# Kernel tuning notes

Hardware: AMD Instinct MI355X
Metric: run time of the kernel (lower is better)

Reference implementation:

```python
import jax, jax.numpy as jnp
import numpy as np

DIM = 128
NUM_HEADS = 8
HEAD_DIM = DIM // NUM_HEADS
N_NODES = 50000
N_EDGES = 800000


def setup_inputs() -> dict:
    key = jax.random.key(0)
    ks = jax.random.split(key, 10)
    scale = 1.0 / np.sqrt(DIM)
    x = jax.random.normal(ks[0], (N_NODES, DIM), dtype=jnp.float32)
    edge_index = jax.random.randint(ks[1], (2, N_EDGES), 0, N_NODES, dtype=jnp.int64)
    Wq = jax.random.normal(ks[2], (DIM, DIM), dtype=jnp.float32) * scale
    bq = jnp.zeros((DIM,), dtype=jnp.float32)
    Wk = jax.random.normal(ks[3], (DIM, DIM), dtype=jnp.float32) * scale
    bk = jnp.zeros((DIM,), dtype=jnp.float32)
    Wv = jax.random.normal(ks[4], (DIM, DIM), dtype=jnp.float32) * scale
    bv = jnp.zeros((DIM,), dtype=jnp.float32)
    Wo = jax.random.normal(ks[5], (DIM, DIM), dtype=jnp.float32) * scale
    bo = jnp.zeros((DIM,), dtype=jnp.float32)
    return {"x": x, "edge_index": edge_index, "Wq": Wq, "bq": bq,
            "Wk": Wk, "bk": bk, "Wv": Wv, "bv": bv, "Wo": Wo, "bo": bo}


def reference(x, edge_index, Wq, bq, Wk, bk, Wv, bv, Wo, bo):
    n = x.shape[0]
    tgt = edge_index[0]  # softmax group / scatter destination
    src = edge_index[1]  # gather source
    # projections: torch nn.Linear -> x @ W.T + b
    q = (x @ Wq.T + bq).reshape(n, NUM_HEADS, HEAD_DIM)
    k = (x @ Wk.T + bk).reshape(n, NUM_HEADS, HEAD_DIM)
    v = (x @ Wv.T + bv).reshape(n, NUM_HEADS, HEAD_DIM)
    # edge-wise attention scores: [E, H]
    scores = jnp.einsum('ehd,ehd->eh', q[src], k[tgt]) / np.sqrt(HEAD_DIM).astype(np.float32)
    # segment softmax over edges grouped by target node
    m = jax.ops.segment_max(scores, tgt, num_segments=n)          # [N, H]
    m = jax.lax.stop_gradient(m)
    p = jnp.exp(scores - m[tgt])                                   # [E, H]
    s = jax.ops.segment_sum(p, tgt, num_segments=n)               # [N, H]
    probs = p / s[tgt]
    # weighted scatter-add of source values
    weighted = v[src] * probs[..., None]                           # [E, H, D]
    agg = jax.ops.segment_sum(weighted, tgt, num_segments=n)      # [N, H, D]
    out = agg.reshape(n, DIM) @ Wo.T + bo
    # dropout is identity in eval mode
    return out
```

## Files before the change

### kernel.cpp

```cpp
#include <hip/hip_runtime.h>
#include <hip/hip_bf16.h>
#include <math.h>

#define NN 50000
#define NE 800000
#define DIM 128
#define NH 8
#define HD 16
#define NTILE 3125
#define TPB 782
#define LROW 136
#define QVROW 256
#define SCAN_B 196

typedef short v8s __attribute__((ext_vector_type(8)));
typedef float v4f __attribute__((ext_vector_type(4)));

__device__ __forceinline__ unsigned pack2(float a, float b) {
    __hip_bfloat162 h = __float22bfloat162_rn(make_float2(a, b));
    return *reinterpret_cast<unsigned*>(&h);
}
__device__ __forceinline__ float blo(unsigned w) { return __uint_as_float(w << 16); }
__device__ __forceinline__ float bhi(unsigned w) { return __uint_as_float(w & 0xffff0000u); }

__device__ __forceinline__ void stage_w_lds(
    const float* __restrict__ Wg, unsigned short* __restrict__ Wl, int tid)
{
#pragma unroll
    for (int it = 0; it < 8; ++it) {
        int chunk = it * 256 + tid;
        int row = chunk >> 4, c8 = chunk & 15;
        float4 f0 = ((const float4*)Wg)[2 * chunk];
        float4 f1 = ((const float4*)Wg)[2 * chunk + 1];
        uint4 o = { pack2(f0.x, f0.y), pack2(f0.z, f0.w),
                    pack2(f1.x, f1.y), pack2(f1.z, f1.w) };
        *(uint4*)(Wl + row * LROW + c8 * 8) = o;
    }
}

__global__ __launch_bounds__(256) void qkv_mfma_kernel(
    const float* __restrict__ x,
    const float* __restrict__ Wq, const float* __restrict__ Wk, const float* __restrict__ Wv,
    const float* __restrict__ bq, const float* __restrict__ bk, const float* __restrict__ bv,
    unsigned short* __restrict__ qvb, unsigned short* __restrict__ kb,
    const int* __restrict__ tgt, int* __restrict__ cnt)
{
    __shared__ unsigned short Wl[DIM * LROW];
    const int mat = blockIdx.x % 3;
    const int tg  = blockIdx.x / 3;
    const int tid = threadIdx.x;
    const int lane = tid & 63;
    const int warp = tid >> 6;
    const int m = lane & 15;
    const int quad = lane >> 4;

    const int gsize = 3 * TPB * 256;
    for (int e = blockIdx.x * 256 + tid; e < NE; e += gsize)
        atomicAdd(cnt + tgt[e], 1);

    const float* Wg = (mat == 0) ? Wq : (mat == 1) ? Wk : Wv;
    stage_w_lds(Wg, Wl, tid);
    __syncthreads();

    const int rt = tg * 4 + warp;
    if (rt >= NTILE) return;
    const int node = rt * 16 + m;

    const float* bias_p = (mat == 0) ? bq : (mat == 1) ? bk : bv;

    v8s a[4];
#pragma unroll
    for (int kt = 0; kt < 4; ++kt) {
        const float4* xr = (const float4*)(x + (size_t)node * DIM + kt * 32 + quad * 8);
        float4 f0 = xr[0], f1 = xr[1];
        uint4 u = { pack2(f0.x, f0.y), pack2(f0.z, f0.w),
                    pack2(f1.x, f1.y), pack2(f1.z, f1.w) };
        a[kt] = *(v8s*)&u;
    }

#pragma unroll
    for (int nt = 0; nt < 8; ++nt) {
        v4f c = {0.f, 0.f, 0.f, 0.f};
#pragma unroll
        for (int kt = 0; kt < 4; ++kt) {
            v8s wf = *(const v8s*)(Wl + (nt * 16 + m) * LROW + kt * 32 + quad * 8);
            c = __builtin_amdgcn_mfma_f32_16x16x32_bf16(wf, a[kt], c, 0, 0, 0);
        }
        const int cbase = nt * 16 + quad * 4;
        float4 b4 = *(const float4*)(bias_p + cbase);
        float o0 = c[0] + b4.x, o1 = c[1] + b4.y;
        float o2 = c[2] + b4.z, o3 = c[3] + b4.w;
        if (mat == 1) {
            uint2 pk = { pack2(o0, o1), pack2(o2, o3) };
            *(uint2*)(kb + (size_t)node * DIM + cbase) = pk;
        } else {
            int p0 = 2 * cbase + ((mat == 2) ? 2 : 0);
            *(unsigned*)(qvb + (size_t)node * QVROW + p0)     = pack2(o0, o1);
            *(unsigned*)(qvb + (size_t)node * QVROW + p0 + 4) = pack2(o2, o3);
        }
    }
}

__global__ __launch_bounds__(256) void scan1_kernel(
    const int* __restrict__ cnt, int* __restrict__ off, int* __restrict__ bsum)
{
    __shared__ int ws4[4];
    const int tid = threadIdx.x, lane = tid & 63, wid = tid >> 6;
    int i = blockIdx.x * 256 + tid;
    int v0 = (i < NN) ? cnt[i] : 0;
    int incl = v0;
#pragma unroll
    for (int d = 1; d < 64; d <<= 1) {
        int t = __shfl_up(incl, d);
        if (lane >= d) incl += t;
    }
    if (lane == 63) ws4[wid] = incl;
    __syncthreads();
    int wexcl = 0;
#pragma unroll
    for (int t = 0; t < 3; ++t) if (t < wid) wexcl += ws4[t];
    if (i < NN) off[i] = wexcl + incl - v0;
    if (tid == 255) bsum[blockIdx.x] = wexcl + incl;
}

__global__ __launch_bounds__(256) void scan23_kernel(
    const int* __restrict__ bsum, int* __restrict__ off, int* __restrict__ cursor)
{
    __shared__ int ws4[4];
    __shared__ int base_s, total_s;
    const int tid = threadIdx.x, lane = tid & 63, wid = tid >> 6;
    int v0 = (tid < SCAN_B) ? bsum[tid] : 0;
    int incl = v0;
#pragma unroll
    for (int d = 1; d < 64; d <<= 1) {
        int t = __shfl_up(incl, d);
        if (lane >= d) incl += t;
    }
    if (lane == 63) ws4[wid] = incl;
    __syncthreads();
    int wexcl = 0;
#pragma unroll
    for (int t = 0; t < 3; ++t) if (t < wid) wexcl += ws4[t];
    int excl = wexcl + incl - v0;
    if (tid == blockIdx.x) base_s = excl;
    if (tid == SCAN_B - 1) total_s = excl + v0;
    __syncthreads();
    int i = blockIdx.x * 256 + tid;
    if (i < NN) {
        int t = off[i] + base_s;
        off[i] = t;
        cursor[i] = t;
    }
    if (blockIdx.x == SCAN_B - 1 && tid == 0) off[NN] = total_s;
}

__global__ __launch_bounds__(256) void fill_kernel(
    const int* __restrict__ tgt, const int* __restrict__ src,
    int* __restrict__ cursor, int* __restrict__ edge_src)
{
    int e = blockIdx.x * 256 + threadIdx.x;
    if (e >= NE) return;
    int t = tgt[e];
    int pos = atomicAdd(cursor + t, 1);
    edge_src[pos] = src[e];
}

__global__ __launch_bounds__(256) void attn_kernel(
    const int* __restrict__ off, const int* __restrict__ edge_src,
    const unsigned short* __restrict__ qvb, const unsigned short* __restrict__ kb,
    unsigned short* __restrict__ aggb)
{
    __shared__ float red[2][64][3];
    const int tid = threadIdx.x;
    const int nib = tid >> 7;
    const int w   = (tid >> 6) & 1;
    const int lane = tid & 63;
    const int node = blockIdx.x * 2 + nib;

    const int base = off[node];
    const int deg  = off[node + 1] - base;

    unsigned kw = *(const unsigned*)(kb + (size_t)node * DIM + 2 * lane);
    const float klo = blo(kw), khi = bhi(kw);

    const int j = lane & 7;
    const int gb = lane & 56;

    float ax = 0.f, ay = 0.f, ss = 0.f;
    const int nw = (deg + 1 - w) >> 1;
    for (int c0 = 0; c0 < nw; c0 += 64) {
        int idx = c0 + lane;
        int srcv = edge_src[base + min(2 * idx + w, deg - 1)];
        int nchunk = min(nw - c0, 64);
        for (int b = 0; b < nchunk; b += 8) {
            int nb = min(nchunk - b, 8);
            uint2 qv[8];
#pragma unroll
            for (int i = 0; i < 8; ++i) {
                int si = __shfl(srcv, b + min(i, nb - 1));
                qv[i] = *(const uint2*)(qvb + (size_t)si * QVROW + 4 * lane);
            }
            float part[8];
#pragma unroll
            for (int i = 0; i < 8; ++i)
                part[i] = blo(qv[i].x) * klo + bhi(qv[i].x) * khi;
            float r1[4];
#pragma unroll
            for (int t = 0; t < 4; ++t) {
                float keep = (j & 1) ? part[2 * t + 1] : part[2 * t];
                float send = (j & 1) ? part[2 * t]     : part[2 * t + 1];
                r1[t] = keep + __shfl_xor(send, 1);
            }
            float r2[2];
#pragma unroll
            for (int u = 0; u < 2; ++u) {
                float keep = (j & 2) ? r1[2 * u + 1] : r1[2 * u];
                float send = (j & 2) ? r1[2 * u]     : r1[2 * u + 1];
                r2[u] = keep + __shfl_xor(send, 2);
            }
            float keep = (j & 4) ? r2[1] : r2[0];
            float send = (j & 4) ? r2[0] : r2[1];
            float tot = keep + __shfl_xor(send, 4);
            float p = __expf(tot * 0.25f);
#pragma unroll
            for (int i = 0; i < 8; ++i) {
                if (i < nb) {
                    float pi = __shfl(p, gb + i);
                    unsigned vv = qv[i].y;
                    ax += pi * blo(vv);
                    ay += pi * bhi(vv);
                    ss += pi;
                }
            }
        }
    }
    if (w == 1) {
        red[nib][lane][0] = ax; red[nib][lane][1] = ay; red[nib][lane][2] = ss;
    }
    __syncthreads();
    if (w == 0) {
        ax += red[nib][lane][0]; ay += red[nib][lane][1]; ss += red[nib][lane][2];
        unsigned* ap = (unsigned*)(aggb + (size_t)node * DIM + 2 * lane);
        if (deg == 0) {
            *ap = 0u;
        } else {
            float inv = 1.f / ss;
            *ap = pack2(ax * inv, ay * inv);
        }
    }
}

__global__ __launch_bounds__(256) void outproj_mfma_kernel(
    const unsigned short* __restrict__ aggb, const float* __restrict__ Wo,
    const float* __restrict__ bo, float* __restrict__ out)
{
    __shared__ unsigned short Wl[DIM * LROW];
    const int tid = threadIdx.x;
    const int lane = tid & 63;
    const int warp = tid >> 6;
    const int m = lane & 15;
    const int quad = lane >> 4;

    stage_w_lds(Wo, Wl, tid);

    const int rt = blockIdx.x * 4 + warp;
    const bool active = (rt < NTILE);
    const int node = (active ? rt : 0) * 16 + m;

    v8s a[4];
    if (active) {
#pragma unroll
        for (int kt = 0; kt < 4; ++kt)
            a[kt] = *(const v8s*)(aggb + (size_t)node * DIM + kt * 32 + quad * 8);
    }
    __syncthreads();
    if (!active) return;

#pragma unroll
    for (int nt = 0; nt < 8; ++nt) {
        v4f c = {0.f, 0.f, 0.f, 0.f};
#pragma unroll
        for (int kt = 0; kt < 4; ++kt) {
            v8s wf = *(const v8s*)(Wl + (nt * 16 + m) * LROW + kt * 32 + quad * 8);
            c = __builtin_amdgcn_mfma_f32_16x16x32_bf16(wf, a[kt], c, 0, 0, 0);
        }
        const int cbase = nt * 16 + quad * 4;
        float4 b4 = *(const float4*)(bo + cbase);
        float4 o = { c[0] + b4.x, c[1] + b4.y, c[2] + b4.z, c[3] + b4.w };
        *(float4*)(out + (size_t)node * DIM + cbase) = o;
    }
}

extern "C" void kernel_launch(void* const* d_in, const int* in_sizes, int n_in,
                              void* d_out, int out_size, void* d_ws, size_t ws_size,
                              hipStream_t stream) {
    const float* x  = (const float*)d_in[0];
    const int*   ei = (const int*)d_in[1];
    const float* Wq = (const float*)d_in[2];
    const float* bq = (const float*)d_in[3];
    const float* Wk = (const float*)d_in[4];
    const float* bk = (const float*)d_in[5];
    const float* Wv = (const float*)d_in[6];
    const float* bv = (const float*)d_in[7];
    const float* Wo = (const float*)d_in[8];
    const float* bo = (const float*)d_in[9];

    const int* tgt = ei;
    const int* src = ei + NE;

    char* ws = (char*)d_ws;
    const size_t SZ_QV = (size_t)NN * QVROW * 2;
    const size_t SZ_BF = (size_t)NN * DIM * 2;

    unsigned short* qvb  = (unsigned short*)(ws);
    unsigned short* kb   = (unsigned short*)(ws + SZ_QV);
    unsigned short* aggb = (unsigned short*)(ws + SZ_QV + SZ_BF);

    char* wi = ws + SZ_QV + 2 * SZ_BF;
    int* cnt      = (int*)(wi);
    int* off      = (int*)(wi + (size_t)NN * 4);
    int* cursor   = (int*)(wi + (size_t)(2 * NN + 1) * 4);
    int* edge_src = (int*)(wi + (size_t)(3 * NN + 1) * 4);
    int* bsum     = (int*)(wi + (size_t)(3 * NN + 1) * 4 + (size_t)NE * 4);

    const int edge_blocks = (NE + 255) / 256;

    hipMemsetAsync(cnt, 0, (size_t)NN * 4, stream);
    qkv_mfma_kernel<<<3 * TPB, 256, 0, stream>>>(
        x, Wq, Wk, Wv, bq, bk, bv, qvb, kb, tgt, cnt);
    scan1_kernel<<<SCAN_B, 256, 0, stream>>>(cnt, off, bsum);
    scan23_kernel<<<SCAN_B, 256, 0, stream>>>(bsum, off, cursor);
    fill_kernel<<<edge_blocks, 256, 0, stream>>>(tgt, src, cursor, edge_src);
    attn_kernel<<<(NN + 1) / 2, 256, 0, stream>>>(off, edge_src, qvb, kb, aggb);
    outproj_mfma_kernel<<<TPB, 256, 0, stream>>>(aggb, Wo, bo, (float*)d_out);
}
```

Baseline: 265.0 us.

## Swap MFMA operand order, reorder block mapping, and specialize full-chunk attention path

The QKV and output-projection MFMAs now swap the A/B operands, so each lane owns one output column across four rows and writes scalar bf16/float values instead of packed vectors. QKV blocks are grouped by matrix (blockIdx/TPB) rather than interleaved. The attention kernel adds a fast path for full 8-edge chunks that drops per-edge bounds checks and accumulates the softmax denominator per lane, reducing it with shuffles at the end. The scalar strided stores may coalesce worse than the earlier vector stores.

```diff
diff --git a/kernel.cpp b/kernel.cpp
--- a/kernel.cpp
+++ b/kernel.cpp
@@ -20,6 +20,9 @@
     __hip_bfloat162 h = __float22bfloat162_rn(make_float2(a, b));
     return *reinterpret_cast<unsigned*>(&h);
 }
+__device__ __forceinline__ unsigned short f2b1(float f) {
+    return (unsigned short)(pack2(f, 0.f) & 0xffffu);
+}
 __device__ __forceinline__ float blo(unsigned w) { return __uint_as_float(w << 16); }
 __device__ __forceinline__ float bhi(unsigned w) { return __uint_as_float(w & 0xffff0000u); }
 
@@ -46,8 +49,8 @@
     const int* __restrict__ tgt, int* __restrict__ cnt)
 {
     __shared__ unsigned short Wl[DIM * LROW];
-    const int mat = blockIdx.x % 3;
-    const int tg  = blockIdx.x / 3;
+    const int mat = blockIdx.x / TPB;
+    const int tg  = blockIdx.x % TPB;
     const int tid = threadIdx.x;
     const int lane = tid & 63;
     const int warp = tid >> 6;
@@ -64,14 +67,14 @@
 
     const int rt = tg * 4 + warp;
     if (rt >= NTILE) return;
-    const int node = rt * 16 + m;
+    const int r0 = rt * 16;
 
     const float* bias_p = (mat == 0) ? bq : (mat == 1) ? bk : bv;
 
     v8s a[4];
 #pragma unroll
     for (int kt = 0; kt < 4; ++kt) {
-        const float4* xr = (const float4*)(x + (size_t)node * DIM + kt * 32 + quad * 8);
+        const float4* xr = (const float4*)(x + (size_t)(r0 + m) * DIM + kt * 32 + quad * 8);
         float4 f0 = xr[0], f1 = xr[1];
         uint4 u = { pack2(f0.x, f0.y), pack2(f0.z, f0.w),
                     pack2(f1.x, f1.y), pack2(f1.z, f1.w) };
@@ -83,20 +86,21 @@
         v4f c = {0.f, 0.f, 0.f, 0.f};
 #pragma unroll
         for (int kt = 0; kt < 4; ++kt) {
-            v8s wf = *(const v8s*)(Wl + (nt * 16 + m) * LROW + kt * 32 + quad * 8);
-            c = __builtin_amdgcn_mfma_f32_16x16x32_bf16(wf, a[kt], c, 0, 0, 0);
-        }
-        const int cbase = nt * 16 + quad * 4;
-        float4 b4 = *(const float4*)(bias_p + cbase);
-        float o0 = c[0] + b4.x, o1 = c[1] + b4.y;
-        float o2 = c[2] + b4.z, o3 = c[3] + b4.w;
-        if (mat == 1) {
-            uint2 pk = { pack2(o0, o1), pack2(o2, o3) };
-            *(uint2*)(kb + (size_t)node * DIM + cbase) = pk;
-        } else {
-            int p0 = 2 * cbase + ((mat == 2) ? 2 : 0);
-            *(unsigned*)(qvb + (size_t)node * QVROW + p0)     = pack2(o0, o1);
-            *(unsigned*)(qvb + (size_t)node * QVROW + p0 + 4) = pack2(o2, o3);
+            v8s b = *(const v8s*)(Wl + (nt * 16 + m) * LROW + kt * 32 + quad * 8);
+            c = __builtin_amdgcn_mfma_f32_16x16x32_bf16(a[kt], b, c, 0, 0, 0);
+        }
+        int col = nt * 16 + m;
+        float bias = bias_p[col];
+#pragma unroll
+        for (int i = 0; i < 4; ++i) {
+            int row = r0 + quad * 4 + i;
+            unsigned short val = f2b1(c[i] + bias);
+            if (mat == 1) {
+                kb[(size_t)row * DIM + col] = val;
+            } else {
+                int pos = (col >> 1) * 4 + (col & 1) + ((mat == 2) ? 2 : 0);
+                qvb[(size_t)row * QVROW + pos] = val;
+            }
         }
     }
 }
@@ -195,10 +199,18 @@
         for (int b = 0; b < nchunk; b += 8) {
             int nb = min(nchunk - b, 8);
             uint2 qv[8];
-#pragma unroll
-            for (int i = 0; i < 8; ++i) {
-                int si = __shfl(srcv, b + min(i, nb - 1));
-                qv[i] = *(const uint2*)(qvb + (size_t)si * QVROW + 4 * lane);
+            if (nb == 8) {
+#pragma unroll
+                for (int i = 0; i < 8; ++i) {
+                    int si = __shfl(srcv, b + i);
+                    qv[i] = *(const uint2*)(qvb + (size_t)si * QVROW + 4 * lane);
+                }
+            } else {
+#pragma unroll
+                for (int i = 0; i < 8; ++i) {
+                    int si = __shfl(srcv, b + min(i, nb - 1));
+                    qv[i] = *(const uint2*)(qvb + (size_t)si * QVROW + 4 * lane);
+                }
             }
             float part[8];
 #pragma unroll
@@ -222,18 +234,33 @@
             float send = (j & 4) ? r2[0] : r2[1];
             float tot = keep + __shfl_xor(send, 4);
             float p = __expf(tot * 0.25f);
-#pragma unroll
-            for (int i = 0; i < 8; ++i) {
-                if (i < nb) {
+            if (nb == 8) {
+                ss += p;
+#pragma unroll
+                for (int i = 0; i < 8; ++i) {
                     float pi = __shfl(p, gb + i);
                     unsigned vv = qv[i].y;
                     ax += pi * blo(vv);
                     ay += pi * bhi(vv);
-                    ss += pi;
                 }
-            }
-        }
-    }
+            } else {
+                if (j < nb) ss += p;
+#pragma unroll
+                for (int i = 0; i < 8; ++i) {
+                    if (i < nb) {
+                        float pi = __shfl(p, gb + i);
+                        unsigned vv = qv[i].y;
+                        ax += pi * blo(vv);
+                        ay += pi * bhi(vv);
+                    }
+                }
+            }
+        }
+    }
+    ss += __shfl_xor(ss, 1);
+    ss += __shfl_xor(ss, 2);
+    ss += __shfl_xor(ss, 4);
+
     if (w == 1) {
         red[nib][lane][0] = ax; red[nib][lane][1] = ay; red[nib][lane][2] = ss;
     }
@@ -265,13 +292,13 @@
 
     const int rt = blockIdx.x * 4 + warp;
     const bool active = (rt < NTILE);
-    const int node = (active ? rt : 0) * 16 + m;
+    const int r0 = (active ? rt : 0) * 16;
 
     v8s a[4];
     if (active) {
 #pragma unroll
         for (int kt = 0; kt < 4; ++kt)
-            a[kt] = *(const v8s*)(aggb + (size_t)node * DIM + kt * 32 + quad * 8);
+            a[kt] = *(const v8s*)(aggb + (size_t)(r0 + m) * DIM + kt * 32 + quad * 8);
     }
     __syncthreads();
     if (!active) return;
@@ -281,13 +308,16 @@
         v4f c = {0.f, 0.f, 0.f, 0.f};
 #pragma unroll
         for (int kt = 0; kt < 4; ++kt) {
-            v8s wf = *(const v8s*)(Wl + (nt * 16 + m) * LROW + kt * 32 + quad * 8);
-            c = __builtin_amdgcn_mfma_f32_16x16x32_bf16(wf, a[kt], c, 0, 0, 0);
-        }
-        const int cbase = nt * 16 + quad * 4;
-        float4 b4 = *(const float4*)(bo + cbase);
-        float4 o = { c[0] + b4.x, c[1] + b4.y, c[2] + b4.z, c[3] + b4.w };
-        *(float4*)(out + (size_t)node * DIM + cbase) = o;
+            v8s b = *(const v8s*)(Wl + (nt * 16 + m) * LROW + kt * 32 + quad * 8);
+            c = __builtin_amdgcn_mfma_f32_16x16x32_bf16(a[kt], b, c, 0, 0, 0);
+        }
+        int col = nt * 16 + m;
+        float bias = bo[col];
+#pragma unroll
+        for (int i = 0; i < 4; ++i) {
+            int row = r0 + quad * 4 + i;
+            out[(size_t)row * DIM + col] = c[i] + bias;
+        }
     }
 }
 
```

After: 268.1 us. Within noise of the previous version (+1.2%).
